# Kernel tuning notes

Measured on AMD Instinct MI355X. Metric: run time of the kernel, lower is better.

## Reference

```python
import jax, jax.numpy as jnp
import numpy as np

B, C, L = 32, 512, 16          # batch, clauses per CNF, max literals per clause
D, H, P = 256, 1024, 16        # clause_hidden_dim, hidden_size, prefix_tokens
NH, NL = 8, 4                  # adapter_heads, adapter_layers
MAXV = 512                     # max_variables


def _ln(x, w, b, eps=1e-5):
    m = jnp.mean(x, axis=-1, keepdims=True)
    v = jnp.mean(jnp.square(x - m), axis=-1, keepdims=True)
    return (x - m) * jax.lax.rsqrt(v + eps) * w + b


def _mha(q, k, v, w_in, b_in, w_out, b_out, nh):
    E = q.shape[-1]
    dh = E // nh
    wq, wk, wv = jnp.split(w_in, 3, axis=0)
    bq, bk, bv = jnp.split(b_in, 3, axis=0)

    def heads(x, w, b):
        y = x @ w.T + b
        return y.reshape(x.shape[0], x.shape[1], nh, dh).transpose(0, 2, 1, 3)

    qh, kh, vh = heads(q, wq, bq), heads(k, wk, bk), heads(v, wv, bv)
    att = jax.nn.softmax(jnp.einsum('bhqd,bhkd->bhqk', qh, kh) * (1.0 / np.sqrt(dh)), axis=-1)
    o = jnp.einsum('bhqk,bhkd->bhqd', att, vh).transpose(0, 2, 1, 3).reshape(q.shape[0], q.shape[1], E)
    return o @ w_out.T + b_out


def setup_inputs() -> dict:
    key = jax.random.key(0)
    ks = jax.random.split(key, 16)
    s = 0.02
    var_idx = jax.random.randint(ks[0], (B, C, L), 0, MAXV + 1)
    sign_idx = jax.random.randint(ks[1], (B, C, L), 1, 3)   # 1=positive literal, 2=negative
    lens = jax.random.randint(ks[2], (B, C), 1, L + 1)      # ragged clause lengths >= 1
    lit_mask = jnp.arange(L)[None, None, :] < lens[..., None]
    inp = dict(var_idx=var_idx, sign_idx=sign_idx, lit_mask=lit_mask)
    inp['var_emb'] = jax.random.normal(ks[3], (MAXV + 1, D)) * s
    inp['sign_emb'] = jax.random.normal(ks[4], (3, D)) * s
    inp['litpos_emb'] = jax.random.normal(ks[5], (L, D)) * s
    inp['clausepos_emb'] = jax.random.normal(ks[6], (C, D)) * s
    inp['enc_in_w'] = jax.random.normal(ks[7], (NL, 3 * D, D)) * s
    inp['enc_in_b'] = jnp.zeros((NL, 3 * D))
    inp['enc_out_w'] = jax.random.normal(ks[8], (NL, D, D)) * s
    inp['enc_out_b'] = jnp.zeros((NL, D))
    inp['enc_ff1_w'] = jax.random.normal(ks[9], (NL, 4 * D, D)) * s
    inp['enc_ff1_b'] = jnp.zeros((NL, 4 * D))
    inp['enc_ff2_w'] = jax.random.normal(ks[10], (NL, D, 4 * D)) * s
    inp['enc_ff2_b'] = jnp.zeros((NL, D))
    inp['enc_n1_w'] = jnp.ones((NL, D))
    inp['enc_n1_b'] = jnp.zeros((NL, D))
    inp['enc_n2_w'] = jnp.ones((NL, D))
    inp['enc_n2_b'] = jnp.zeros((NL, D))
    inp['th_ln_w'] = jnp.ones((D,))
    inp['th_ln_b'] = jnp.zeros((D,))
    inp['th_w'] = jax.random.normal(ks[11], (H, D)) * s
    inp['th_b'] = jnp.zeros((H,))
    inp['pq'] = jax.random.normal(ks[12], (P, H))
    inp['pa_in_w'] = jax.random.normal(ks[13], (3 * H, H)) * s
    inp['pa_in_b'] = jnp.zeros((3 * H,))
    inp['pa_out_w'] = jax.random.normal(ks[14], (H, H)) * s
    inp['pa_out_b'] = jnp.zeros((H,))
    inp['pn_w'] = jnp.ones((H,))
    inp['pn_b'] = jnp.zeros((H,))
    return inp


def reference(var_idx, sign_idx, lit_mask, var_emb, sign_emb, litpos_emb, clausepos_emb,
              enc_in_w, enc_in_b, enc_out_w, enc_out_b, enc_ff1_w, enc_ff1_b,
              enc_ff2_w, enc_ff2_b, enc_n1_w, enc_n1_b, enc_n2_w, enc_n2_b,
              th_ln_w, th_ln_b, th_w, th_b, pq, pa_in_w, pa_in_b, pa_out_w, pa_out_b,
              pn_w, pn_b):
    # literal states [B,C,L,D]: four embedding gathers fused into one expression
    lit = (var_emb[var_idx] + sign_emb[sign_idx]
           + litpos_emb[None, None, :, :] + clausepos_emb[None, :, None, :])
    m = lit_mask[..., None].astype(lit.dtype)
    x = jnp.sum(lit * m, axis=2) / jnp.sum(m, axis=2)   # masked mean-pool -> [B,C,D]
    for i in range(NL):  # PyTorch post-norm TransformerEncoderLayer, gelu (exact)
        a = _mha(x, x, x, enc_in_w[i], enc_in_b[i], enc_out_w[i], enc_out_b[i], NH)
        x = _ln(x + a, enc_n1_w[i], enc_n1_b[i])
        f = jax.nn.gelu(x @ enc_ff1_w[i].T + enc_ff1_b[i], approximate=False) @ enc_ff2_w[i].T + enc_ff2_b[i]
        x = _ln(x + f, enc_n2_w[i], enc_n2_b[i])
    ch = _ln(x, th_ln_w, th_ln_b) @ th_w.T + th_b       # to_hidden -> [B,C,H]
    q = jnp.broadcast_to(pq[None], (ch.shape[0], P, H))
    pref = _mha(q, ch, ch, pa_in_w, pa_in_b, pa_out_w, pa_out_b, NH)
    return _ln(pref + q, pn_w, pn_b)                    # [B,P,H]
```

## Files before the change

### kernel.cpp

```cpp
#include <hip/hip_runtime.h>
#include <hip/hip_bf16.h>

typedef unsigned short u16;
typedef unsigned int u32;
typedef __attribute__((ext_vector_type(8))) short short8;
typedef __attribute__((ext_vector_type(4))) float floatx4;

#define BB 32
#define CC 512
#define LL 16
#define DD 256
#define HH 1024
#define PP 16
#define NLAY 4

__device__ __forceinline__ float bf2f(u16 u) {
  u32 x = ((u32)u) << 16; float f; __builtin_memcpy(&f, &x, 4); return f;
}
__device__ __forceinline__ u16 f2bf(float f) {
  __hip_bfloat16 h = __float2bfloat16(f);
  u16 r; __builtin_memcpy(&r, &h, 2); return r;
}
__device__ __forceinline__ void gload_lds16(const u16* g, u16* l) {
  __builtin_amdgcn_global_load_lds(
      (const __attribute__((address_space(1))) void*)g,
      (__attribute__((address_space(3))) void*)l, 16, 0, 0);
}

__global__ __launch_bounds__(256) void cvt_kernel(
    const float* __restrict__ s0, const float* __restrict__ s1,
    const float* __restrict__ s2, const float* __restrict__ s3,
    const float* __restrict__ s4, const float* __restrict__ s5,
    const float* __restrict__ s6, const float* __restrict__ s7,
    const float* __restrict__ s8, const float* __restrict__ s9,
    const float* __restrict__ s10, const float* __restrict__ s11,
    u16* __restrict__ dst)
{
  const float* srcs[12] = {s0, s1, s2, s3, s4, s5, s6, s7, s8, s9, s10, s11};
  const int pfx[12] = {786432, 1048576, 2097152, 3145728, 3407872, 6553600, 7602176,
                       7618560, 7749888, 7750656, 7754752, 7885824};
  int e = (blockIdx.x * 256 + threadIdx.x) * 4;
  int seg = 0;
  while (e >= pfx[seg]) seg++;
  int start = seg ? pfx[seg - 1] : 0;
  float4 f = *(const float4*)(srcs[seg] + (e - start));
  u16 o[4] = {f2bf(f.x), f2bf(f.y), f2bf(f.z), f2bf(f.w)};
  *(uint2*)(dst + e) = *(const uint2*)o;
}

__global__ __launch_bounds__(256) void thwT_kernel(
    const float* __restrict__ thw, u16* __restrict__ out)
{
  __shared__ float tile[32][33];
  int bx = blockIdx.x & 7, by = blockIdx.x >> 3;
  int tx = threadIdx.x & 31, ty = threadIdx.x >> 5;
  #pragma unroll
  for (int i = 0; i < 4; ++i) {
    int h = by * 32 + ty + i * 8, d = bx * 32 + tx;
    tile[ty + i * 8][tx] = thw[h * 256 + d];
  }
  __syncthreads();
  #pragma unroll
  for (int i = 0; i < 4; ++i) {
    int d = bx * 32 + ty + i * 8, h = by * 32 + tx;
    out[d * 1024 + h] = f2bf(tile[tx][ty + i * 8]);
  }
}

__global__ __launch_bounds__(256) void biasfold_kernel(
    const u16* __restrict__ Wkv, const float* __restrict__ thb,
    const float* __restrict__ paib, float* __restrict__ out)
{
  int wv = threadIdx.x >> 6, lane = threadIdx.x & 63;
  int n = blockIdx.x * 4 + wv;
  const u16* wr = Wkv + (size_t)n * 1024;
  float s = 0.f;
  #pragma unroll
  for (int i = 0; i < 16; ++i) {
    int h = i * 64 + lane;
    s += bf2f(wr[h]) * thb[h];
  }
  #pragma unroll
  for (int off = 32; off; off >>= 1) s += __shfl_xor(s, off);
  if (!lane) out[n] = s + paib[1024 + n];
}

__global__ __launch_bounds__(256) void redk_kernel(
    const float* __restrict__ part, const float* __restrict__ bias,
    const float* __restrict__ res, float* __restrict__ outf, u16* __restrict__ outb,
    int N, int nz, int total, int flags)
{
  int idx = (blockIdx.x * 256 + threadIdx.x) * 4;
  if (idx >= total) return;
  float4 a = *(const float4*)(part + idx);
  for (int z = 1; z < nz; ++z) {
    float4 b = *(const float4*)(part + (size_t)z * total + idx);
    a.x += b.x; a.y += b.y; a.z += b.z; a.w += b.w;
  }
  int row = idx / N, col = idx - row * N;
  float v4[4] = {a.x, a.y, a.z, a.w};
  #pragma unroll
  for (int i = 0; i < 4; ++i) {
    if (bias) v4[i] += bias[col + i];
    if (res) v4[i] += res[(size_t)((flags & 4) ? (row & 15) : row) * N + col + i];
  }
  if (outf) {
    *(float4*)(outf + idx) = *(const float4*)v4;
  } else {
    u16 o[4] = {f2bf(v4[0]), f2bf(v4[1]), f2bf(v4[2]), f2bf(v4[3])};
    *(uint2*)(outb + idx) = *(const uint2*)o;
  }
}

__global__ __launch_bounds__(256) void embed_kernel(
    const int* __restrict__ vi, const int* __restrict__ si, const int* __restrict__ mk,
    const u16* __restrict__ veb, const u16* __restrict__ seb,
    const u16* __restrict__ lpeb, const u16* __restrict__ cpeb,
    u16* __restrict__ xb)
{
  int t = threadIdx.x;
  int bc = blockIdx.x * 2 + (t >> 7);
  int c = bc & (CC - 1);
  int dl = (t & 127) * 2;
  int base = bc * LL;
  float a0 = 0.f, a1 = 0.f; int cnt = 0;
  #pragma unroll
  for (int l = 0; l < LL; ++l) {
    if (mk[base + l]) {
      int v = vi[base + l], s = si[base + l];
      u32 vv = *(const u32*)&veb[v * DD + dl];
      u32 sv = *(const u32*)&seb[s * DD + dl];
      u32 lv = *(const u32*)&lpeb[l * DD + dl];
      a0 += bf2f((u16)vv) + bf2f((u16)sv) + bf2f((u16)lv);
      a1 += bf2f((u16)(vv >> 16)) + bf2f((u16)(sv >> 16)) + bf2f((u16)(lv >> 16));
      cnt++;
    }
  }
  u32 cv = *(const u32*)&cpeb[c * DD + dl];
  float inv = 1.f / (float)cnt;
  u32 pk = (u32)f2bf(a0 * inv + bf2f((u16)cv)) | ((u32)f2bf(a1 * inv + bf2f((u16)(cv >> 16))) << 16);
  *(u32*)&xb[(size_t)bc * DD + dl] = pk;
}

template<int NC, bool GELU, bool LN, bool DLN>
__global__ __launch_bounds__(256) void gwide_kernel(
    const u16* __restrict__ A, const u16* __restrict__ W, const float* __restrict__ bias,
    const u16* __restrict__ resb, const float* __restrict__ gam, const float* __restrict__ bet,
    const float* __restrict__ gam2, const float* __restrict__ bet2,
    u16* __restrict__ out, int N, int K)
{
  constexpr int NT = NC / 32;
  __shared__ __align__(16) u16 As[32 * 64];
  __shared__ __align__(16) u16 Ws[NC * 64];
  __shared__ float sred[32][2][2];
  __shared__ float sred2[32][2][2];
  int t = threadIdx.x, lane = t & 63, w = t >> 6;
  int wm = w & 1, wn = w >> 1;
  int mrow = lane & 15, quad = lane >> 4;
  int bn0 = blockIdx.x * NC, bm0 = blockIdx.y * 32;

  int rA = t >> 3, gcA = (t & 7) ^ (rA & 7);
  const u16* gAp = A + (size_t)(bm0 + rA) * K + gcA * 8;
  u16* lAp = As + (w * 64) * 8;
  const u16* gW0 = W + (size_t)(bn0 + rA) * K + gcA * 8;
  u16* lW0 = Ws + (w * 64) * 8;

  floatx4 acc[NT];
  #pragma unroll
  for (int nt = 0; nt < NT; ++nt) acc[nt] = (floatx4){0.f, 0.f, 0.f, 0.f};

  for (int k0 = 0; k0 < K; k0 += 64) {
    __syncthreads();
    gload_lds16(gAp, lAp); gAp += 64;
    #pragma unroll
    for (int i = 0; i < NT; ++i)
      gload_lds16(gW0 + (size_t)i * 32 * K, lW0 + i * 2048);
    gW0 += 64;
    __syncthreads();
    #pragma unroll
    for (int ks = 0; ks < 2; ++ks) {
      int sw = ((ks * 4 + quad) ^ (mrow & 7)) * 8;
      short8 af = *(const short8*)&As[(wm * 16 + mrow) * 64 + sw];
      #pragma unroll
      for (int nt = 0; nt < NT; ++nt) {
        int rw = wn * (NC / 2) + nt * 16 + mrow;
        short8 bf = *(const short8*)&Ws[rw * 64 + sw];
        acc[nt] = __builtin_amdgcn_mfma_f32_16x16x32_bf16(af, bf, acc[nt], 0, 0, 0);
      }
    }
  }

  if constexpr (LN) {
    float val[NT][4];
    float bv[NT];
    #pragma unroll
    for (int nt = 0; nt < NT; ++nt) bv[nt] = bias[wn * 128 + nt * 16 + mrow];
    #pragma unroll
    for (int r = 0; r < 4; ++r) {
      int gm = bm0 + wm * 16 + quad * 4 + r;
      float sr = 0.f, s2r = 0.f;
      #pragma unroll
      for (int nt = 0; nt < NT; ++nt) {
        int gn = wn * 128 + nt * 16 + mrow;
        float v = acc[nt][r] + bv[nt] + bf2f(resb[(size_t)gm * 256 + gn]);
        val[nt][r] = v; sr += v; s2r += v * v;
      }
      sr += __shfl_xor(sr, 1); s2r += __shfl_xor(s2r, 1);
      sr += __shfl_xor(sr, 2); s2r += __shfl_xor(s2r, 2);
      sr += __shfl_xor(sr, 4); s2r += __shfl_xor(s2r, 4);
      sr += __shfl_xor(sr, 8); s2r += __shfl_xor(s2r, 8);
      if (mrow == 0) { sred[wm * 16 + quad * 4 + r][wn][0] = sr; sred[wm * 16 + quad * 4 + r][wn][1] = s2r; }
    }
    __syncthreads();
    #pragma unroll
    for (int r = 0; r < 4; ++r) {
      int lrow = wm * 16 + quad * 4 + r;
      float S = sred[lrow][0][0] + sred[lrow][1][0];
      float S2 = sred[lrow][0][1] + sred[lrow][1][1];
      float mean = S * (1.f / 256.f);
      float var = S2 * (1.f / 256.f) - mean * mean;
      float inv = rsqrtf(var + 1e-5f);
      float sr2 = 0.f, s2r2 = 0.f;
      #pragma unroll
      for (int nt = 0; nt < NT; ++nt) {
        int gn = wn * 128 + nt * 16 + mrow;
        float y = (val[nt][r] - mean) * inv * gam[gn] + bet[gn];
        val[nt][r] = y;
        if constexpr (DLN) { sr2 += y; s2r2 += y * y; }
        else out[(size_t)(bm0 + lrow) * 256 + gn] = f2bf(y);
      }
      if constexpr (DLN) {
        sr2 += __shfl_xor(sr2, 1); s2r2 += __shfl_xor(s2r2, 1);
        sr2 += __shfl_xor(sr2, 2); s2r2 += __shfl_xor(s2r2, 2);
        sr2 += __shfl_xor(sr2, 4); s2r2 += __shfl_xor(s2r2, 4);
        sr2 += __shfl_xor(sr2, 8); s2r2 += __shfl_xor(s2r2, 8);
        if (mrow == 0) { sred2[lrow][wn][0] = sr2; sred2[lrow][wn][1] = s2r2; }
      }
    }
    if constexpr (DLN) {
      __syncthreads();
      #pragma unroll
      for (int r = 0; r < 4; ++r) {
        int lrow = wm * 16 + quad * 4 + r;
        float S = sred2[lrow][0][0] + sred2[lrow][1][0];
        float S2 = sred2[lrow][0][1] + sred2[lrow][1][1];
        float mean = S * (1.f / 256.f);
        float var = S2 * (1.f / 256.f) - mean * mean;
        float inv = rsqrtf(var + 1e-5f);
        #pragma unroll
        for (int nt = 0; nt < NT; ++nt) {
          int gn = wn * 128 + nt * 16 + mrow;
          float z = (val[nt][r] - mean) * inv * gam2[gn] + bet2[gn];
          out[(size_t)(bm0 + lrow) * 256 + gn] = f2bf(z);
        }
      }
    }
  } else {
    #pragma unroll
    for (int nt = 0; nt < NT; ++nt) {
      int gn = bn0 + wn * (NC / 2) + nt * 16 + mrow;
      float bv = bias[gn];
      #pragma unroll
      for (int r = 0; r < 4; ++r) {
        int gm = bm0 + wm * 16 + quad * 4 + r;
        float v = acc[nt][r] + bv;
        if (GELU) v = 0.5f * v * (1.f + erff(v * 0.70710678118654752f));
        out[(size_t)gm * N + gn] = f2bf(v);
      }
    }
  }
}

__global__ __launch_bounds__(256) void gemm128s_kernel(
    const u16* __restrict__ A, const u16* __restrict__ W, const float* __restrict__ bias,
    u16* __restrict__ kb, u16* __restrict__ vtp,
    const u16* __restrict__ pqA, const u16* __restrict__ Wq, const float* __restrict__ biasq,
    u16* __restrict__ qh, int K)
{
  __shared__ __align__(16) u16 SH[16384];
  u16* As = SH;
  u16* Bs = SH + 8192;
  int t = threadIdx.x, lane = t & 63, w = t >> 6;
  int wm = w & 1, wn = w >> 1;
  int mrow = lane & 15, quad = lane >> 4;
  int id = blockIdx.x;
  int c, bm0, bn0;
  const u16* Abase; const u16* Wbase;
  int KK;
  if (id < 8) {
    c = -1; bm0 = 0; bn0 = id * 128;
    Abase = pqA; Wbase = Wq;
    KK = 1024;
  } else {
    int id2 = id - 8;
    int g = id2 >> 6, w6 = id2 & 63;
    int r4 = (w6 & 7) >> 1;
    c = ((w6 >> 3) << 1) | (w6 & 1);
    bm0 = (g * 4 + r4) * 128;
    bn0 = c * 128;
    Abase = A; Wbase = W;
    KK = K;
  }

  const u16* gA[4]; const u16* gB[4];
  u16* lA[4]; u16* lB[4];
  #pragma unroll
  for (int it = 0; it < 4; ++it) {
    int cc = w * 256 + it * 64 + lane;
    int r = cc >> 3;
    int gc = (cc & 7) ^ (r & 7);
    gA[it] = Abase + (size_t)(bm0 + r) * KK + gc * 8;
    gB[it] = Wbase + (size_t)(bn0 + r) * KK + gc * 8;
    lA[it] = As + (w * 256 + it * 64) * 8;
    lB[it] = Bs + (w * 256 + it * 64) * 8;
  }
  floatx4 acc[4][4];
  #pragma unroll
  for (int i = 0; i < 4; ++i)
    #pragma unroll
    for (int j = 0; j < 4; ++j)
      acc[i][j] = (floatx4){0.f, 0.f, 0.f, 0.f};
  int sw0 = ((0 * 4 + quad) ^ (mrow & 7)) * 8;
  int sw1 = ((1 * 4 + quad) ^ (mrow & 7)) * 8;

  for (int k0 = 0; k0 < KK; k0 += 64) {
    __syncthreads();
    #pragma unroll
    for (int it = 0; it < 4; ++it) { gload_lds16(gA[it], lA[it]); gA[it] += 64; }
    #pragma unroll
    for (int it = 0; it < 4; ++it) { gload_lds16(gB[it], lB[it]); gB[it] += 64; }
    __syncthreads();
    #pragma unroll
    for (int ks = 0; ks < 2; ++ks) {
      int sw = ks ? sw1 : sw0;
      short8 af[4], bfr[4];
      #pragma unroll
      for (int mi = 0; mi < 4; ++mi)
        af[mi] = *(const short8*)&As[(wm * 64 + mi * 16 + mrow) * 64 + sw];
      #pragma unroll
      for (int nj = 0; nj < 4; ++nj)
        bfr[nj] = *(const short8*)&Bs[(wn * 64 + nj * 16 + mrow) * 64 + sw];
      #pragma unroll
      for (int mi = 0; mi < 4; ++mi)
        #pragma unroll
        for (int nj = 0; nj < 4; ++nj)
          acc[mi][nj] = __builtin_amdgcn_mfma_f32_16x16x32_bf16(af[mi], bfr[nj], acc[mi][nj], 0, 0, 0);
    }
  }

  if (c == -1) {
    if (wm == 0) {
      #pragma unroll
      for (int nj = 0; nj < 4; ++nj) {
        int gn = bn0 + wn * 64 + nj * 16 + mrow;
        float bv = biasq[gn];
        #pragma unroll
        for (int r = 0; r < 4; ++r) {
          int gm = quad * 4 + r;
          qh[(size_t)gm * 1024 + gn] = f2bf(acc[0][nj][r] + bv);
        }
      }
    }
  } else if (c < 8) {
    #pragma unroll
    for (int nj = 0; nj < 4; ++nj) {
      int gn = bn0 + wn * 64 + nj * 16 + mrow;
      float bv = bias[gn];
      #pragma unroll
      for (int mi = 0; mi < 4; ++mi)
        #pragma unroll
        for (int r = 0; r < 4; ++r) {
          int gm = bm0 + wm * 64 + mi * 16 + quad * 4 + r;
          kb[(size_t)gm * 1024 + gn] = f2bf(acc[mi][nj][r] + bv);
        }
    }
  } else {
    int h = c - 8;
    int b = bm0 >> 9, jt = (bm0 >> 7) & 3;
    size_t basev = ((size_t)(b * 8 + h) * 128) * 512 + jt * 128;
    #pragma unroll
    for (int pass = 0; pass < 2; ++pass) {
      __syncthreads();
      if (wn == pass) {
        #pragma unroll
        for (int nj = 0; nj < 4; ++nj) {
          int dl = nj * 16 + mrow;
          float bv = bias[bn0 + pass * 64 + dl];
          #pragma unroll
          for (int mi = 0; mi < 4; ++mi) {
            int jp = quad * 32 + wm * 4 + mi;
            #pragma unroll
            for (int r = 0; r < 4; ++r)
              SH[dl * 136 + jp + r * 8] = f2bf(acc[mi][nj][r] + bv);
          }
        }
      }
      __syncthreads();
      #pragma unroll
      for (int i = 0; i < 4; ++i) {
        int idx = t + i * 256;
        int d = idx >> 4, jc4 = (idx & 15) * 8;
        uint4 v = *(const uint4*)&SH[d * 136 + jc4];
        *(uint4*)(vtp + basev + (size_t)(pass * 64 + d) * 512 + jc4) = v;
      }
    }
  }
}

__global__ __launch_bounds__(256) void gemm128_kernel(
    const u16* __restrict__ A, const u16* __restrict__ W, const float* __restrict__ bias,
    const float* __restrict__ res, void* __restrict__ out,
    int M, int N, int K, int flags)
{
  __shared__ __align__(16) u16 As[128 * 64];
  __shared__ __align__(16) u16 Bs[128 * 64];
  int t = threadIdx.x;
  int lane = t & 63, w = t >> 6;
  int wm = w & 1, wn = w >> 1;
  int bn0 = blockIdx.x * 128, bm0 = blockIdx.y * 128;
  int mrow = lane & 15, quad = lane >> 4;
  int z = blockIdx.z, NZ = gridDim.z;
  int Kc = K / NZ, kbase = z * Kc;

  const u16* gA[4]; const u16* gB[4];
  u16* lA[4]; u16* lB[4];
  #pragma unroll
  for (int it = 0; it < 4; ++it) {
    int c = w * 256 + it * 64 + lane;
    int r = c >> 3;
    int gc = (c & 7) ^ (r & 7);
    gA[it] = A + (size_t)(bm0 + r) * K + kbase + gc * 8;
    gB[it] = W + (size_t)(bn0 + r) * K + kbase + gc * 8;
    lA[it] = As + (w * 256 + it * 64) * 8;
    lB[it] = Bs + (w * 256 + it * 64) * 8;
  }
  floatx4 acc[4][4];
  #pragma unroll
  for (int i = 0; i < 4; ++i)
    #pragma unroll
    for (int j = 0; j < 4; ++j)
      acc[i][j] = (floatx4){0.f, 0.f, 0.f, 0.f};
  int sw0 = ((0 * 4 + quad) ^ (mrow & 7)) * 8;
  int sw1 = ((1 * 4 + quad) ^ (mrow & 7)) * 8;

  for (int k0 = 0; k0 < Kc; k0 += 64) {
    __syncthreads();
    #pragma unroll
    for (int it = 0; it < 4; ++it) { gload_lds16(gA[it], lA[it]); gA[it] += 64; }
    #pragma unroll
    for (int it = 0; it < 4; ++it) { gload_lds16(gB[it], lB[it]); gB[it] += 64; }
    __syncthreads();
    #pragma unroll
    for (int ks = 0; ks < 2; ++ks) {
      int sw = ks ? sw1 : sw0;
      short8 af[4], bfr[4];
      #pragma unroll
      for (int mi = 0; mi < 4; ++mi)
        af[mi] = *(const short8*)&As[(wm * 64 + mi * 16 + mrow) * 64 + sw];
      #pragma unroll
      for (int nj = 0; nj < 4; ++nj)
        bfr[nj] = *(const short8*)&Bs[(wn * 64 + nj * 16 + mrow) * 64 + sw];
      #pragma unroll
      for (int mi = 0; mi < 4; ++mi)
        #pragma unroll
        for (int nj = 0; nj < 4; ++nj)
          acc[mi][nj] = __builtin_amdgcn_mfma_f32_16x16x32_bf16(af[mi], bfr[nj], acc[mi][nj], 0, 0, 0);
    }
  }
  if (NZ > 1) {
    float* po = (float*)out + (size_t)z * M * N;
    #pragma unroll
    for (int nj = 0; nj < 4; ++nj) {
      int gn = bn0 + wn * 64 + nj * 16 + mrow;
      #pragma unroll
      for (int mi = 0; mi < 4; ++mi)
        #pragma unroll
        for (int r = 0; r < 4; ++r) {
          int gm = bm0 + wm * 64 + mi * 16 + quad * 4 + r;
          po[(size_t)gm * N + gn] = acc[mi][nj][r];
        }
    }
    return;
  }
  bool do_gelu = (flags & 1) != 0, of32 = (flags & 2) != 0;
  #pragma unroll
  for (int nj = 0; nj < 4; ++nj) {
    int gn = bn0 + wn * 64 + nj * 16 + mrow;
    float bv = bias ? bias[gn] : 0.f;
    #pragma unroll
    for (int mi = 0; mi < 4; ++mi) {
      #pragma unroll
      for (int r = 0; r < 4; ++r) {
        int gm = bm0 + wm * 64 + mi * 16 + quad * 4 + r;
        float v = acc[mi][nj][r] + bv;
        if (do_gelu) v = 0.5f * v * (1.f + erff(v * 0.70710678118654752f));
        if (flags & 4) v += res[(size_t)(gm & 15) * N + gn];
        else if (res) v += res[(size_t)gm * N + gn];
        if (of32) ((float*)out)[(size_t)gm * N + gn] = v;
        else      ((u16*)out)[(size_t)gm * N + gn] = f2bf(v);
      }
    }
  }
}

template<int D>
__global__ __launch_bounds__(256) void lnw_kernel(
    const float* __restrict__ in, const float* __restrict__ w, const float* __restrict__ b,
    float* __restrict__ outf, u16* __restrict__ outb)
{
  constexpr int NV = D / 64;
  int lane = threadIdx.x & 63, wv = threadIdx.x >> 6;
  int row = blockIdx.x * 4 + wv;
  const float* xr = in + (size_t)row * D;
  float v[NV];
  float s = 0.f, s2 = 0.f;
  #pragma unroll
  for (int i = 0; i < NV; ++i) {
    v[i] = xr[lane + i * 64];
    s += v[i]; s2 += v[i] * v[i];
  }
  #pragma unroll
  for (int off = 32; off > 0; off >>= 1) { s += __shfl_xor(s, off); s2 += __shfl_xor(s2, off); }
  float mean = s / (float)D;
  float var = s2 / (float)D - mean * mean;
  float inv = rsqrtf(var + 1e-5f);
  #pragma unroll
  for (int i = 0; i < NV; ++i) {
    int col = lane + i * 64;
    float y = (v[i] - mean) * inv * w[col] + b[col];
    size_t o = (size_t)row * D + col;
    if (outf) outf[o] = y;
    if (outb) outb[o] = f2bf(y);
  }
}

__global__ __launch_bounds__(256, 5) void attn_enc6_kernel(
    const u16* __restrict__ qkv, u16* __restrict__ out)
{
  __shared__ __align__(16) u16 Ks[64 * 40];
  __shared__ __align__(16) u16 Vt[32 * 72];
  __shared__ __align__(16) u16 Pl[4 * 32 * 72];
  int F = blockIdx.x;
  int xcd = F & 7, jj = F >> 3;
  int pair = xcd * 32 + (jj >> 2), qt = jj & 3;
  int b = pair >> 3, h = pair & 7;
  int t = threadIdx.x, lane = t & 63, w = t >> 6;
  int mrow = lane & 15, quad = lane >> 4;
  int q0 = qt * 128 + w * 32;
  short8 qf[2];
  #pragma unroll
  for (int mi = 0; mi < 2; ++mi)
    qf[mi] = *(const short8*)(qkv + (size_t)(b * CC + q0 + mi * 16 + mrow) * 768 + h * 32 + quad * 8);
  floatx4 o[2][2];
  #pragma unroll
  for (int mi = 0; mi < 2; ++mi)
    #pragma unroll
    for (int di = 0; di < 2; ++di) o[mi][di] = (floatx4){0.f, 0.f, 0.f, 0.f};
  float lst[2][4] = {{0.f,0.f,0.f,0.f},{0.f,0.f,0.f,0.f}};
  const float sc = 0.17677669529663687f * 1.4426950408889634f;
  const floatx4 zf = (floatx4){0.f, 0.f, 0.f, 0.f};
  for (int jt = 0; jt < 8; ++jt) {
    if (jt) __syncthreads();
    {
      int j = t >> 2, q4 = (t & 3) * 8;
      uint4 kk = *(const uint4*)(qkv + (size_t)(b * CC + jt * 64 + j) * 768 + 256 + h * 32 + q4);
      *(uint4*)&Ks[j * 40 + q4] = kk;
      uint4 vv = *(const uint4*)(qkv + (size_t)(b * CC + jt * 64 + j) * 768 + 512 + h * 32 + q4);
      u16 tmp[8]; *(uint4*)tmp = vv;
      int jp = (j & 15) * 4 + (j >> 4);
      #pragma unroll
      for (int i = 0; i < 8; ++i) Vt[(q4 + i) * 72 + jp] = tmp[i];
    }
    __syncthreads();
    floatx4 s[2][4];
    #pragma unroll
    for (int nj = 0; nj < 4; ++nj) {
      short8 bf = *(const short8*)&Ks[(nj * 16 + mrow) * 40 + quad * 8];
      s[0][nj] = __builtin_amdgcn_mfma_f32_16x16x32_bf16(qf[0], bf, zf, 0, 0, 0);
      s[1][nj] = __builtin_amdgcn_mfma_f32_16x16x32_bf16(qf[1], bf, zf, 0, 0, 0);
    }
    #pragma unroll
    for (int mi = 0; mi < 2; ++mi) {
      #pragma unroll
      for (int r = 0; r < 4; ++r) {
        float ps = 0.f; u16 hv[4];
        #pragma unroll
        for (int nj = 0; nj < 4; ++nj) {
          float p = exp2f(s[mi][nj][r] * sc);
          ps += p; hv[nj] = f2bf(p);
        }
        lst[mi][r] += ps;
        *(uint2*)&Pl[(w * 32 + mi * 16 + quad * 4 + r) * 72 + mrow * 4] = *(uint2*)hv;
      }
    }
    #pragma unroll
    for (int ks = 0; ks < 2; ++ks) {
      short8 a0 = *(const short8*)&Pl[(w * 32 + mrow) * 72 + ks * 32 + quad * 8];
      short8 a1 = *(const short8*)&Pl[(w * 32 + 16 + mrow) * 72 + ks * 32 + quad * 8];
      short8 b0 = *(const short8*)&Vt[mrow * 72 + ks * 32 + quad * 8];
      short8 b1 = *(const short8*)&Vt[(16 + mrow) * 72 + ks * 32 + quad * 8];
      o[0][0] = __builtin_amdgcn_mfma_f32_16x16x32_bf16(a0, b0, o[0][0], 0, 0, 0);
      o[0][1] = __builtin_amdgcn_mfma_f32_16x16x32_bf16(a0, b1, o[0][1], 0, 0, 0);
      o[1][0] = __builtin_amdgcn_mfma_f32_16x16x32_bf16(a1, b0, o[1][0], 0, 0, 0);
      o[1][1] = __builtin_amdgcn_mfma_f32_16x16x32_bf16(a1, b1, o[1][1], 0, 0, 0);
    }
  }
  #pragma unroll
  for (int mi = 0; mi < 2; ++mi) {
    #pragma unroll
    for (int r = 0; r < 4; ++r) {
      float l = lst[mi][r];
      l += __shfl_xor(l, 1); l += __shfl_xor(l, 2);
      l += __shfl_xor(l, 4); l += __shfl_xor(l, 8);
      float inv = 1.f / l;
      int row = b * CC + q0 + mi * 16 + quad * 4 + r;
      #pragma unroll
      for (int di = 0; di < 2; ++di)
        out[(size_t)row * DD + h * 32 + di * 16 + mrow] = f2bf(o[mi][di][r] * inv);
    }
  }
}

__global__ __launch_bounds__(256) void attn_pref2_kernel(
    const u16* __restrict__ qh, const u16* __restrict__ kb, const u16* __restrict__ vtp,
    u16* __restrict__ out)
{
  __shared__ __align__(16) u16 Pl[4 * 16 * 136];
  __shared__ float Ored[4 * 16 * 128];
  __shared__ float Lred[4 * 16];
  int h = blockIdx.x, b = blockIdx.y;
  int t = threadIdx.x, lane = t & 63, w = t >> 6;
  int mrow = lane & 15, quad = lane >> 4;
  const float sc = 0.08838834764831845f * 1.4426950408889634f;
  const floatx4 zf = (floatx4){0.f, 0.f, 0.f, 0.f};
  short8 qf[4];
  #pragma unroll
  for (int ks = 0; ks < 4; ++ks)
    qf[ks] = *(const short8*)(qh + mrow * HH + h * 128 + ks * 32 + quad * 8);
  const u16* kbase = kb + ((size_t)(b * CC + w * 128)) * 1024 + h * 128;
  floatx4 s[8];
  #pragma unroll
  for (int nj = 0; nj < 8; ++nj) {
    floatx4 a = zf;
    #pragma unroll
    for (int ks = 0; ks < 4; ++ks) {
      short8 kf = *(const short8*)(kbase + (size_t)(nj * 16 + mrow) * 1024 + ks * 32 + quad * 8);
      a = __builtin_amdgcn_mfma_f32_16x16x32_bf16(qf[ks], kf, a, 0, 0, 0);
    }
    s[nj] = a;
  }
  #pragma unroll
  for (int r = 0; r < 4; ++r) {
    float ps = 0.f; u16 hv[8];
    #pragma unroll
    for (int nj = 0; nj < 8; ++nj) {
      float p = exp2f(s[nj][r] * sc);
      ps += p; hv[nj] = f2bf(p);
    }
    ps += __shfl_xor(ps, 1); ps += __shfl_xor(ps, 2);
    ps += __shfl_xor(ps, 4); ps += __shfl_xor(ps, 8);
    if (mrow == 0) Lred[w * 16 + quad * 4 + r] = ps;
    *(uint4*)&Pl[(w * 16 + quad * 4 + r) * 136 + mrow * 8] = *(uint4*)hv;
  }
  short8 pa[4];
  #pragma unroll
  for (int ks = 0; ks < 4; ++ks)
    pa[ks] = *(const short8*)&Pl[(w * 16 + mrow) * 136 + ks * 32 + quad * 8];
  const u16* vbase = vtp + ((size_t)(b * 8 + h) * 128) * 512 + w * 128;
  floatx4 o[8];
  #pragma unroll
  for (int nd = 0; nd < 8; ++nd) o[nd] = zf;
  #pragma unroll
  for (int nd = 0; nd < 8; ++nd) {
    #pragma unroll
    for (int ks = 0; ks < 4; ++ks) {
      short8 vf = *(const short8*)(vbase + (size_t)(nd * 16 + mrow) * 512 + ks * 32 + quad * 8);
      o[nd] = __builtin_amdgcn_mfma_f32_16x16x32_bf16(pa[ks], vf, o[nd], 0, 0, 0);
    }
  }
  #pragma unroll
  for (int nd = 0; nd < 8; ++nd)
    #pragma unroll
    for (int r = 0; r < 4; ++r)
      Ored[(w * 16 + quad * 4 + r) * 128 + nd * 16 + mrow] = o[nd][r];
  __syncthreads();
  int row = t >> 4, d0 = (t & 15) * 8;
  float l = Lred[row] + Lred[16 + row] + Lred[32 + row] + Lred[48 + row];
  float inv = 1.f / l;
  u16 ov[8];
  #pragma unroll
  for (int i = 0; i < 8; ++i) {
    int d = d0 + i;
    float sum = Ored[row * 128 + d] + Ored[(16 + row) * 128 + d]
              + Ored[(32 + row) * 128 + d] + Ored[(48 + row) * 128 + d];
    ov[i] = f2bf(sum * inv);
  }
  *(uint4*)(out + ((size_t)(b * PP + row)) * HH + h * 128 + d0) = *(const uint4*)ov;
}

extern "C" void kernel_launch(void* const* d_in, const int* in_sizes, int n_in,
                              void* d_out, int out_size, void* d_ws, size_t ws_size,
                              hipStream_t stream)
{
  const int* vi = (const int*)d_in[0];
  const int* si = (const int*)d_in[1];
  const int* mk = (const int*)d_in[2];
  const float* ve   = (const float*)d_in[3];
  const float* se   = (const float*)d_in[4];
  const float* lpe  = (const float*)d_in[5];
  const float* cpe  = (const float*)d_in[6];
  const float* eiw  = (const float*)d_in[7];
  const float* eib  = (const float*)d_in[8];
  const float* eow  = (const float*)d_in[9];
  const float* eob  = (const float*)d_in[10];
  const float* f1w  = (const float*)d_in[11];
  const float* f1b  = (const float*)d_in[12];
  const float* f2w  = (const float*)d_in[13];
  const float* f2b  = (const float*)d_in[14];
  const float* n1w  = (const float*)d_in[15];
  const float* n1b  = (const float*)d_in[16];
  const float* n2w  = (const float*)d_in[17];
  const float* n2b  = (const float*)d_in[18];
  const float* tlw  = (const float*)d_in[19];
  const float* tlb  = (const float*)d_in[20];
  const float* thw  = (const float*)d_in[21];
  const float* thb  = (const float*)d_in[22];
  const float* pq   = (const float*)d_in[23];
  const float* paiw = (const float*)d_in[24];
  const float* paib = (const float*)d_in[25];
  const float* paow = (const float*)d_in[26];
  const float* paob = (const float*)d_in[27];
  const float* pnw  = (const float*)d_in[28];
  const float* pnb  = (const float*)d_in[29];

  const int NROW = BB * CC;
  const size_t MB = 1048576;
  char* base = (char*)d_ws;
  u16* xb   = (u16*)(base);
  u16* qkvb = (u16*)(base + 8 * MB);
  u16* atto = (u16*)(base + 32 * MB);
  u16* h1   = (u16*)(base + 8 * MB);
  u16* tln  = (u16*)(base + 96 * MB);
  u16* kb   = (u16*)(base);
  u16* vtp  = (u16*)(base + 32 * MB);
  u16* wcb   = (u16*)(base + 64 * MB);
  u16* thwTb = (u16*)(base + 65 * MB);
  float* bkv = (float*)(base + 66 * MB);
  float* skpart = (float*)(base + 80 * MB);
  u16* wbf  = (u16*)(base + 104 * MB);
  u16* qh    = (u16*)(base + 120 * MB);
  u16* prefo = qh + 32768;
  float* prefout = (float*)(base + 122 * MB);

  u16* eiw_b  = wbf + 0;
  u16* eow_b  = wbf + 786432;
  u16* f1w_b  = wbf + 1048576;
  u16* f2w_b  = wbf + 2097152;
  u16* thw_b  = wbf + 3145728;
  u16* paiw_b = wbf + 3407872;
  u16* paow_b = wbf + 6553600;
  u16* pqb    = wbf + 7602176;
  u16* veb    = wbf + 7618560;
  u16* seb    = wbf + 7749888;
  u16* lpeb   = wbf + 7750656;
  u16* cpeb   = wbf + 7754752;

  dim3 blk(256);
  cvt_kernel<<<7701, blk, 0, stream>>>(eiw, eow, f1w, f2w, thw, paiw, paow, pq,
                                       ve, se, lpe, cpe, wbf);
  thwT_kernel<<<256, blk, 0, stream>>>(thw, thwTb);
  biasfold_kernel<<<512, blk, 0, stream>>>(paiw_b + (size_t)HH * HH, thb, paib, bkv);
  gemm128_kernel<<<dim3(2, 16, 4), blk, 0, stream>>>(
      paiw_b + (size_t)HH * HH, thwTb, nullptr, nullptr, skpart, 2048, 256, HH, 0);
  redk_kernel<<<512, blk, 0, stream>>>(skpart, nullptr, nullptr, nullptr, wcb,
                                       256, 4, 2048 * 256, 0);
  embed_kernel<<<NROW/2, blk, 0, stream>>>(vi, si, mk, veb, seb, lpeb, cpeb, xb);
  for (int i = 0; i < NLAY; ++i) {
    gwide_kernel<384, false, false, false><<<dim3(2, NROW/32), blk, 0, stream>>>(
        xb, eiw_b + (size_t)i*768*DD, eib + i*768, nullptr, nullptr, nullptr, nullptr, nullptr,
        qkvb, 768, DD);
    attn_enc6_kernel<<<1024, blk, 0, stream>>>(qkvb, atto);
    gwide_kernel<256, false, true, false><<<dim3(1, NROW/32), blk, 0, stream>>>(
        atto, eow_b + (size_t)i*DD*DD, eob + i*DD, xb, n1w + i*DD, n1b + i*DD, nullptr, nullptr,
        xb, DD, DD);
    gwide_kernel<256, true, false, false><<<dim3(4, NROW/32), blk, 0, stream>>>(
        xb, f1w_b + (size_t)i*HH*DD, f1b + i*HH, nullptr, nullptr, nullptr, nullptr, nullptr,
        h1, HH, DD);
    if (i < NLAY - 1) {
      gwide_kernel<256, false, true, false><<<dim3(1, NROW/32), blk, 0, stream>>>(
          h1, f2w_b + (size_t)i*DD*HH, f2b + i*DD, xb, n2w + i*DD, n2b + i*DD, nullptr, nullptr,
          xb, DD, HH);
    } else {
      gwide_kernel<256, false, true, true><<<dim3(1, NROW/32), blk, 0, stream>>>(
          h1, f2w_b + (size_t)i*DD*HH, f2b + i*DD, xb, n2w + i*DD, n2b + i*DD, tlw, tlb,
          tln, DD, HH);
    }
  }
  gemm128s_kernel<<<2056, blk, 0, stream>>>(
      tln, wcb, bkv, kb, vtp,
      pqb, paiw_b, paib, qh, DD);
  attn_pref2_kernel<<<dim3(8, BB), blk, 0, stream>>>(qh, kb, vtp, prefo);
  gemm128_kernel<<<dim3(1024/128, (BB*PP)/128, 4), blk, 0, stream>>>(
      prefo, paow_b, nullptr, nullptr, skpart, BB*PP, HH, HH, 0);
  redk_kernel<<<512, blk, 0, stream>>>(skpart, paob, pq, prefout, nullptr,
                                       1024, 4, BB*PP*HH, 4);
  lnw_kernel<1024><<<(BB*PP)/4, blk, 0, stream>>>(prefout, pnw, pnb, (float*)d_out, nullptr);
}
```

Baseline: 672.4 us.

## Fold prefix K/V projections into attention via associativity over pooled clause states

```diff
diff --git a/kernel.cpp b/kernel.cpp
--- a/kernel.cpp
+++ b/kernel.cpp
@@ -65,6 +65,50 @@
     int d = bx * 32 + ty + i * 8, h = by * 32 + tx;
     out[d * 1024 + h] = f2bf(tile[tx][ty + i * 8]);
   }
+}
+
+__global__ __launch_bounds__(256) void bT_kernel(
+    const u16* __restrict__ in, u16* __restrict__ out)
+{
+  __shared__ u16 tile[32][33];
+  int bx = blockIdx.x & 7, by = blockIdx.x >> 3;
+  int tx = threadIdx.x & 31, ty = threadIdx.x >> 5;
+  #pragma unroll
+  for (int i = 0; i < 4; ++i) {
+    int hd = by * 32 + ty + i * 8, c = bx * 32 + tx;
+    tile[ty + i * 8][tx] = in[hd * 256 + c];
+  }
+  __syncthreads();
+  #pragma unroll
+  for (int i = 0; i < 4; ++i) {
+    int c = bx * 32 + ty + i * 8, hd = by * 32 + tx;
+    out[c * 1024 + hd] = tile[tx][ty + i * 8];
+  }
+}
+
+__global__ __launch_bounds__(256) void qc_kernel(
+    const u16* __restrict__ qh, const u16* __restrict__ wckT, u16* __restrict__ qcg)
+{
+  int h = blockIdx.x;
+  int t = threadIdx.x, lane = t & 63, w = t >> 6;
+  int mrow = lane & 15, quad = lane >> 4;
+  const floatx4 zf = (floatx4){0.f, 0.f, 0.f, 0.f};
+  floatx4 acc[4] = {zf, zf, zf, zf};
+  #pragma unroll
+  for (int kk = 0; kk < 4; ++kk) {
+    short8 af = *(const short8*)(qh + (size_t)mrow * 1024 + h * 128 + kk * 32 + quad * 8);
+    #pragma unroll
+    for (int ct = 0; ct < 4; ++ct) {
+      int c = w * 64 + ct * 16 + mrow;
+      short8 bf = *(const short8*)(wckT + (size_t)c * 1024 + h * 128 + kk * 32 + quad * 8);
+      acc[ct] = __builtin_amdgcn_mfma_f32_16x16x32_bf16(af, bf, acc[ct], 0, 0, 0);
+    }
+  }
+  #pragma unroll
+  for (int ct = 0; ct < 4; ++ct)
+    #pragma unroll
+    for (int r = 0; r < 4; ++r)
+      qcg[((size_t)h * 16 + quad * 4 + r) * 256 + w * 64 + ct * 16 + mrow] = f2bf(acc[ct][r]);
 }
 
 __global__ __launch_bounds__(256) void biasfold_kernel(
@@ -374,36 +418,6 @@
           kb[(size_t)gm * 1024 + gn] = f2bf(acc[mi][nj][r] + bv);
         }
     }
-  } else {
-    int h = c - 8;
-    int b = bm0 >> 9, jt = (bm0 >> 7) & 3;
-    size_t basev = ((size_t)(b * 8 + h) * 128) * 512 + jt * 128;
-    #pragma unroll
-    for (int pass = 0; pass < 2; ++pass) {
-      __syncthreads();
-      if (wn == pass) {
-        #pragma unroll
-        for (int nj = 0; nj < 4; ++nj) {
-          int dl = nj * 16 + mrow;
-          float bv = bias[bn0 + pass * 64 + dl];
-          #pragma unroll
-          for (int mi = 0; mi < 4; ++mi) {
-            int jp = quad * 32 + wm * 4 + mi;
-            #pragma unroll
-            for (int r = 0; r < 4; ++r)
-              SH[dl * 136 + jp + r * 8] = f2bf(acc[mi][nj][r] + bv);
-          }
-        }
-      }
-      __syncthreads();
-      #pragma unroll
-      for (int i = 0; i < 4; ++i) {
-        int idx = t + i * 256;
-        int d = idx >> 4, jc4 = (idx & 15) * 8;
-        uint4 v = *(const uint4*)&SH[d * 136 + jc4];
-        *(uint4*)(vtp + basev + (size_t)(pass * 64 + d) * 512 + jc4) = v;
-      }
-    }
   }
 }
 
@@ -621,81 +635,104 @@
   }
 }
 
-__global__ __launch_bounds__(256) void attn_pref2_kernel(
-    const u16* __restrict__ qh, const u16* __restrict__ kb, const u16* __restrict__ vtp,
+__global__ __launch_bounds__(256) void attn_preff_kernel(
+    const u16* __restrict__ tln, const u16* __restrict__ wcb,
+    const u16* __restrict__ qcg, const float* __restrict__ bkv,
     u16* __restrict__ out)
 {
-  __shared__ __align__(16) u16 Pl[4 * 16 * 136];
-  __shared__ float Ored[4 * 16 * 128];
-  __shared__ float Lred[4 * 16];
+  __shared__ __align__(16) u16 Ajc[64 * 264];
+  __shared__ __align__(16) u16 Acj[256 * 72];
+  __shared__ __align__(16) u16 Qs[16 * 264];
+  __shared__ __align__(16) u16 Ps[16 * 72];
+  __shared__ __align__(16) u16 Ts[16 * 264];
+  __shared__ float Lred[4][16];
   int h = blockIdx.x, b = blockIdx.y;
   int t = threadIdx.x, lane = t & 63, w = t >> 6;
   int mrow = lane & 15, quad = lane >> 4;
   const float sc = 0.08838834764831845f * 1.4426950408889634f;
   const floatx4 zf = (floatx4){0.f, 0.f, 0.f, 0.f};
-  short8 qf[4];
-  #pragma unroll
-  for (int ks = 0; ks < 4; ++ks)
-    qf[ks] = *(const short8*)(qh + mrow * HH + h * 128 + ks * 32 + quad * 8);
-  const u16* kbase = kb + ((size_t)(b * CC + w * 128)) * 1024 + h * 128;
-  floatx4 s[8];
-  #pragma unroll
-  for (int nj = 0; nj < 8; ++nj) {
-    floatx4 a = zf;
-    #pragma unroll
-    for (int ks = 0; ks < 4; ++ks) {
-      short8 kf = *(const short8*)(kbase + (size_t)(nj * 16 + mrow) * 1024 + ks * 32 + quad * 8);
-      a = __builtin_amdgcn_mfma_f32_16x16x32_bf16(qf[ks], kf, a, 0, 0, 0);
-    }
-    s[nj] = a;
-  }
+  {
+    int q = t >> 4, c0 = (t & 15) * 16;
+    *(uint4*)&Qs[q * 264 + c0]     = *(const uint4*)(qcg + ((size_t)h * 16 + q) * 256 + c0);
+    *(uint4*)&Qs[q * 264 + c0 + 8] = *(const uint4*)(qcg + ((size_t)h * 16 + q) * 256 + c0 + 8);
+  }
+  floatx4 Tacc[4] = {zf, zf, zf, zf};
+  float lacc = 0.f;
+  const u16* tb = tln + (size_t)b * 512 * 256;
+  for (int jt = 0; jt < 8; ++jt) {
+    __syncthreads();
+    {
+      int j = t >> 2, c0 = (t & 3) * 64;
+      #pragma unroll
+      for (int u = 0; u < 8; ++u) {
+        uint4 v = *(const uint4*)(tb + (size_t)(jt * 64 + j) * 256 + c0 + u * 8);
+        *(uint4*)&Ajc[j * 264 + c0 + u * 8] = v;
+        u16 tmp[8]; *(uint4*)tmp = v;
+        #pragma unroll
+        for (int i = 0; i < 8; ++i) Acj[(c0 + u * 8 + i) * 72 + j] = tmp[i];
+      }
+    }
+    __syncthreads();
+    floatx4 s = zf;
+    #pragma unroll
+    for (int kk = 0; kk < 8; ++kk) {
+      short8 af = *(const short8*)&Ajc[(w * 16 + mrow) * 264 + kk * 32 + quad * 8];
+      short8 bf = *(const short8*)&Qs[mrow * 264 + kk * 32 + quad * 8];
+      s = __builtin_amdgcn_mfma_f32_16x16x32_bf16(af, bf, s, 0, 0, 0);
+    }
+    u16 hv[4]; float ps = 0.f;
+    #pragma unroll
+    for (int r = 0; r < 4; ++r) {
+      float p = exp2f(s[r] * sc);
+      ps += p; hv[r] = f2bf(p);
+    }
+    ps += __shfl_xor(ps, 16); ps += __shfl_xor(ps, 32);
+    lacc += ps;
+    *(uint2*)&Ps[mrow * 72 + w * 16 + quad * 4] = *(uint2*)hv;
+    __syncthreads();
+    #pragma unroll
+    for (int kk = 0; kk < 2; ++kk) {
+      short8 af = *(const short8*)&Ps[mrow * 72 + kk * 32 + quad * 8];
+      #pragma unroll
+      for (int ct = 0; ct < 4; ++ct) {
+        short8 bf = *(const short8*)&Acj[(w * 64 + ct * 16 + mrow) * 72 + kk * 32 + quad * 8];
+        Tacc[ct] = __builtin_amdgcn_mfma_f32_16x16x32_bf16(af, bf, Tacc[ct], 0, 0, 0);
+      }
+    }
+  }
+  if (lane < 16) Lred[w][lane] = lacc;
+  __syncthreads();
   #pragma unroll
   for (int r = 0; r < 4; ++r) {
-    float ps = 0.f; u16 hv[8];
-    #pragma unroll
-    for (int nj = 0; nj < 8; ++nj) {
-      float p = exp2f(s[nj][r] * sc);
-      ps += p; hv[nj] = f2bf(p);
-    }
-    ps += __shfl_xor(ps, 1); ps += __shfl_xor(ps, 2);
-    ps += __shfl_xor(ps, 4); ps += __shfl_xor(ps, 8);
-    if (mrow == 0) Lred[w * 16 + quad * 4 + r] = ps;
-    *(uint4*)&Pl[(w * 16 + quad * 4 + r) * 136 + mrow * 8] = *(uint4*)hv;
-  }
-  short8 pa[4];
-  #pragma unroll
-  for (int ks = 0; ks < 4; ++ks)
-    pa[ks] = *(const short8*)&Pl[(w * 16 + mrow) * 136 + ks * 32 + quad * 8];
-  const u16* vbase = vtp + ((size_t)(b * 8 + h) * 128) * 512 + w * 128;
-  floatx4 o[8];
-  #pragma unroll
-  for (int nd = 0; nd < 8; ++nd) o[nd] = zf;
-  #pragma unroll
-  for (int nd = 0; nd < 8; ++nd) {
-    #pragma unroll
-    for (int ks = 0; ks < 4; ++ks) {
-      short8 vf = *(const short8*)(vbase + (size_t)(nd * 16 + mrow) * 512 + ks * 32 + quad * 8);
-      o[nd] = __builtin_amdgcn_mfma_f32_16x16x32_bf16(pa[ks], vf, o[nd], 0, 0, 0);
-    }
-  }
-  #pragma unroll
-  for (int nd = 0; nd < 8; ++nd)
-    #pragma unroll
-    for (int r = 0; r < 4; ++r)
-      Ored[(w * 16 + quad * 4 + r) * 128 + nd * 16 + mrow] = o[nd][r];
+    int q = quad * 4 + r;
+    float l = Lred[0][q] + Lred[1][q] + Lred[2][q] + Lred[3][q];
+    float inv = 1.f / l;
+    #pragma unroll
+    for (int ct = 0; ct < 4; ++ct)
+      Ts[q * 264 + w * 64 + ct * 16 + mrow] = f2bf(Tacc[ct][r] * inv);
+  }
   __syncthreads();
-  int row = t >> 4, d0 = (t & 15) * 8;
-  float l = Lred[row] + Lred[16 + row] + Lred[32 + row] + Lred[48 + row];
-  float inv = 1.f / l;
-  u16 ov[8];
-  #pragma unroll
-  for (int i = 0; i < 8; ++i) {
-    int d = d0 + i;
-    float sum = Ored[row * 128 + d] + Ored[(16 + row) * 128 + d]
-              + Ored[(32 + row) * 128 + d] + Ored[(48 + row) * 128 + d];
-    ov[i] = f2bf(sum * inv);
-  }
-  *(uint4*)(out + ((size_t)(b * PP + row)) * HH + h * 128 + d0) = *(const uint4*)ov;
+  const u16* wv = wcb + (size_t)(1024 + h * 128) * 256;
+  floatx4 oacc[2] = {zf, zf};
+  #pragma unroll
+  for (int kk = 0; kk < 8; ++kk) {
+    short8 af = *(const short8*)&Ts[mrow * 264 + kk * 32 + quad * 8];
+    #pragma unroll
+    for (int dt = 0; dt < 2; ++dt) {
+      short8 bf = *(const short8*)(wv + (size_t)(w * 32 + dt * 16 + mrow) * 256 + kk * 32 + quad * 8);
+      oacc[dt] = __builtin_amdgcn_mfma_f32_16x16x32_bf16(af, bf, oacc[dt], 0, 0, 0);
+    }
+  }
+  #pragma unroll
+  for (int dt = 0; dt < 2; ++dt) {
+    int d = w * 32 + dt * 16 + mrow;
+    float bv = bkv[1024 + h * 128 + d];
+    #pragma unroll
+    for (int r = 0; r < 4; ++r) {
+      int q = quad * 4 + r;
+      out[((size_t)(b * 16 + q)) * 1024 + h * 128 + d] = f2bf(oacc[dt][r] + bv);
+    }
+  }
 }
 
 extern "C" void kernel_launch(void* const* d_in, const int* in_sizes, int n_in,
@@ -741,11 +778,11 @@
   u16* atto = (u16*)(base + 32 * MB);
   u16* h1   = (u16*)(base + 8 * MB);
   u16* tln  = (u16*)(base + 96 * MB);
-  u16* kb   = (u16*)(base);
-  u16* vtp  = (u16*)(base + 32 * MB);
   u16* wcb   = (u16*)(base + 64 * MB);
   u16* thwTb = (u16*)(base + 65 * MB);
   float* bkv = (float*)(base + 66 * MB);
+  u16* wckT  = (u16*)(base + 67 * MB);
+  u16* qcg   = (u16*)(base + 68 * MB);
   float* skpart = (float*)(base + 80 * MB);
   u16* wbf  = (u16*)(base + 104 * MB);
   u16* qh    = (u16*)(base + 120 * MB);
@@ -774,6 +811,10 @@
       paiw_b + (size_t)HH * HH, thwTb, nullptr, nullptr, skpart, 2048, 256, HH, 0);
   redk_kernel<<<512, blk, 0, stream>>>(skpart, nullptr, nullptr, nullptr, wcb,
                                        256, 4, 2048 * 256, 0);
+  gemm128s_kernel<<<8, blk, 0, stream>>>(
+      nullptr, nullptr, nullptr, nullptr, nullptr, pqb, paiw_b, paib, qh, DD);
+  bT_kernel<<<256, blk, 0, stream>>>(wcb, wckT);
+  qc_kernel<<<8, blk, 0, stream>>>(qh, wckT, qcg);
   embed_kernel<<<NROW/2, blk, 0, stream>>>(vi, si, mk, veb, seb, lpeb, cpeb, xb);
   for (int i = 0; i < NLAY; ++i) {
     gwide_kernel<384, false, false, false><<<dim3(2, NROW/32), blk, 0, stream>>>(
@@ -796,10 +837,7 @@
           tln, DD, HH);
     }
   }
-  gemm128s_kernel<<<2056, blk, 0, stream>>>(
-      tln, wcb, bkv, kb, vtp,
-      pqb, paiw_b, paib, qh, DD);
-  attn_pref2_kernel<<<dim3(8, BB), blk, 0, stream>>>(qh, kb, vtp, prefo);
+  attn_preff_kernel<<<dim3(8, BB), blk, 0, stream>>>(tln, wcb, qcg, bkv, prefo);
   gemm128_kernel<<<dim3(1024/128, (BB*PP)/128, 4), blk, 0, stream>>>(
       prefo, paow_b, nullptr, nullptr, skpart, BB*PP, HH, HH, 0);
   redk_kernel<<<512, blk, 0, stream>>>(skpart, paob, pq, prefout, nullptr,
```

Result: no change. 669.4 us (-0.4%).
